# Kernel optimization log

Measured on AMD Instinct MI355X. Metric: run time of the kernel, lower is better.

The kernel has to match this reference:

```python
import jax, jax.numpy as jnp
import numpy as np

N, D, V = 4096, 256, 32000
B, T = 32, 256
U_DECAY, X_DECAY = 0.97, 0.97
EPS = 1e-6


def layernorm_row(z):
    # matches torch: (z - mean) / (std + eps), std with Bessel correction (ddof=1)
    m = jnp.mean(z, axis=-1, keepdims=True)
    s = jnp.std(z, axis=-1, keepdims=True, ddof=1)
    return (z - m) / (s + EPS)


def setup_inputs() -> dict:
    key = jax.random.key(0)
    k1, k2, k3, k4, k5 = jax.random.split(key, 5)
    token_emb = jax.random.normal(k1, (V, D), jnp.float32) / np.float32(np.sqrt(D))
    E = jax.random.normal(k2, (D, N), jnp.float32) / np.float32(np.sqrt(N))
    Dx = jax.random.normal(k3, (N, D), jnp.float32) / np.float32(np.sqrt(D))
    Dy = jax.random.normal(k4, (N, D), jnp.float32) / np.float32(np.sqrt(D))
    idx = jax.random.randint(k5, (B, T), 0, V)
    return {"idx": idx, "token_emb": token_emb, "E": E, "Dx": Dx, "Dy": Dy}


def reference(idx, token_emb, E, Dx, Dy):
    b = idx.shape[0]

    def step(carry, tok):
        x, rho = carry                                   # x: (b,n), rho: (b,d,n)
        v_prev = token_emb[tok]                          # (b,d) embedding gather
        x_t = X_DECAY * x + jax.nn.relu(v_prev @ Dx.T)   # (b,n)
        x_t = x_t / (jnp.sum(jnp.abs(x_t), axis=-1, keepdims=True) + EPS)  # L1 normalize
        a_star = jnp.einsum('bdn,bn->bd', rho, x_t)      # fast-weight readout
        y_t = jax.nn.relu(layernorm_row(a_star) @ Dy.T) * jax.nn.relu(x_t)  # (b,n)
        v_star = layernorm_row(y_t @ E.T)                # (b,d)
        # Hebbian decayed outer-product memory update
        rho = U_DECAY * (rho + jnp.einsum('bd,bn->bdn', layernorm_row(v_prev), x_t))
        return (x_t, rho), v_star

    x0 = jnp.zeros((b, N), jnp.float32)
    rho0 = jnp.zeros((b, D, N), jnp.float32)
    (_, _), vs = jax.lax.scan(step, (x0, rho0), idx.T)   # vs: (T,b,d)
    return jnp.transpose(vs, (1, 0, 2))                  # (b,T,d)
```

## Files before the change

kernel.cpp:

```cpp
#include <hip/hip_runtime.h>
#include <hip/hip_bf16.h>

#define NN 4096
#define DD 256
#define BB 32
#define TT 256
#define EPS 1e-6f
#define DECAY 0.97f
#define LOG2_DECAY -0.043943348f

typedef __hip_bfloat16 bf16;
typedef short short8 __attribute__((ext_vector_type(8)));
typedef float floatx4 __attribute__((ext_vector_type(4)));

__device__ __forceinline__ float blk_sum_256(float v, volatile float* s4) {
#pragma unroll
    for (int o = 32; o > 0; o >>= 1) v += __shfl_down(v, o, 64);
    int lane = threadIdx.x & 63, w = threadIdx.x >> 6;
    __syncthreads();
    if (lane == 0) s4[w] = v;
    __syncthreads();
    return s4[0] + s4[1] + s4[2] + s4[3];
}

__device__ __forceinline__ void gl16(const bf16* g, bf16* l) {
    __builtin_amdgcn_global_load_lds((const __attribute__((address_space(1))) void*)g,
                                     (__attribute__((address_space(3))) void*)l, 16, 0, 0);
}

__global__ void k_detect(const unsigned short* __restrict__ raw, int* __restrict__ flag) {
    __shared__ int cnt[4];
    int tid = threadIdx.x;
    int bad = 0;
    for (int i = tid; i < 8192; i += 256) {
        unsigned int u = raw[2 * i];
        float v = __uint_as_float(u << 16);
        if (!(fabsf(v) < 1e6f)) bad++;
    }
#pragma unroll
    for (int o = 32; o > 0; o >>= 1) bad += __shfl_down(bad, o, 64);
    int lane = tid & 63, w = tid >> 6;
    if (lane == 0) cnt[w] = bad;
    __syncthreads();
    if (tid == 0) flag[0] = (cnt[0] + cnt[1] + cnt[2] + cnt[3] < 32) ? 1 : 0;
}

__global__ void k_convert_bf16(const void* __restrict__ src, bf16* __restrict__ dst, int n,
                               const int* __restrict__ flag) {
    int i = blockIdx.x * 256 + threadIdx.x;
    if (i >= n) return;
    float v = flag[0] ? __bfloat162float(((const bf16*)src)[i]) : ((const float*)src)[i];
    dst[i] = __float2bfloat16(v);
}

__global__ __launch_bounds__(256) void k_gather_ln(const void* __restrict__ emb,
                                                   const int* __restrict__ idx,
                                                   bf16* __restrict__ Vpb,
                                                   bf16* __restrict__ Ub,
                                                   const int* __restrict__ flag) {
    __shared__ float s4[4];
    int r = blockIdx.x, d = threadIdx.x;
    int tok = idx[r];
    long o = (long)tok * DD + d;
    float e = flag[0] ? __bfloat162float(((const bf16*)emb)[o]) : ((const float*)emb)[o];
    Vpb[(long)r * DD + d] = __float2bfloat16(e);
    float m = blk_sum_256(e, s4) * (1.0f / DD);
    float zc = e - m;
    float var = blk_sum_256(zc * zc, s4) * (1.0f / (DD - 1));
    Ub[(long)r * DD + d] = __float2bfloat16(zc / (sqrtf(fmaxf(var, 0.f)) + EPS));
}

__global__ __launch_bounds__(256) void k_transpose(const bf16* __restrict__ Ub,
                                                   bf16* __restrict__ Ut) {
    __shared__ bf16 tile[32][33];
    int b = blockIdx.z;
    int t0 = blockIdx.x * 32, d0 = blockIdx.y * 32;
    const bf16* src = Ub + (long)b * TT * DD;
    bf16* dst = Ut + (long)b * DD * TT;
    int rr = threadIdx.x >> 3, c4 = (threadIdx.x & 7) * 4;
#pragma unroll
    for (int i = 0; i < 4; i++) tile[rr][c4 + i] = src[(long)(t0 + rr) * DD + d0 + c4 + i];
    __syncthreads();
#pragma unroll
    for (int i = 0; i < 4; i++) dst[(long)(d0 + rr) * TT + t0 + c4 + i] = tile[c4 + i][rr];
}

enum { EPI_RELU_BF16 = 0, EPI_NONE_F32 = 1, EPI_RELU_MULX_BF16 = 2 };

template <int EPI, int KSPLIT>
__global__ __launch_bounds__(256) void k_mfma_nt(int K,
                                                 const bf16* __restrict__ A, int lda, long sA,
                                                 const bf16* __restrict__ B, int ldb, long sB,
                                                 void* __restrict__ Cv, int ldc, long sC,
                                                 const bf16* __restrict__ Xaux) {
    __shared__ bf16 As[128][32];
    __shared__ bf16 Bs[128][32];
    int z = blockIdx.z;
    int bz = z / KSPLIT, ks = z % KSPLIT;
    A += (long)bz * sA;
    B += (long)bz * sB;
    int bm = blockIdx.y * 128, bn = blockIdx.x * 128;
    int tid = threadIdx.x;
    int srow = tid >> 2, scol = (tid & 3) << 3;
    int w = tid >> 6, lane = tid & 63;
    int wm = (w >> 1) * 64, wn = (w & 1) * 64;
    int lm = lane & 15, kh = lane >> 4;

    floatx4 acc[4][4];
#pragma unroll
    for (int i = 0; i < 4; i++)
#pragma unroll
        for (int j = 0; j < 4; j++) acc[i][j] = (floatx4){0.f, 0.f, 0.f, 0.f};

    int kchunk = K / KSPLIT;
    int kbeg = ks * kchunk, kend = kbeg + kchunk;
    const bf16* gA0 = A + (long)(bm + srow) * lda + scol;
    const bf16* gA1 = gA0 + (long)64 * lda;
    const bf16* gB0 = B + (long)(bn + srow) * ldb + scol;
    const bf16* gB1 = gB0 + (long)64 * ldb;
    bf16* lA0 = &As[srow][scol];
    bf16* lA1 = &As[srow + 64][scol];
    bf16* lB0 = &Bs[srow][scol];
    bf16* lB1 = &Bs[srow + 64][scol];

    for (int k0 = kbeg; k0 < kend; k0 += 32) {
        __syncthreads();
        gl16(gA0 + k0, lA0);
        gl16(gA1 + k0, lA1);
        gl16(gB0 + k0, lB0);
        gl16(gB1 + k0, lB1);
        __syncthreads();
        short8 af[4], bfr[4];
#pragma unroll
        for (int i = 0; i < 4; i++) af[i] = *(const short8*)&As[wm + i * 16 + lm][kh * 8];
#pragma unroll
        for (int j = 0; j < 4; j++) bfr[j] = *(const short8*)&Bs[wn + j * 16 + lm][kh * 8];
#pragma unroll
        for (int i = 0; i < 4; i++)
#pragma unroll
            for (int j = 0; j < 4; j++)
                acc[i][j] = __builtin_amdgcn_mfma_f32_16x16x32_bf16(af[i], bfr[j], acc[i][j], 0, 0, 0);
    }

    long cbase = (long)z * sC;
#pragma unroll
    for (int i = 0; i < 4; i++) {
#pragma unroll
        for (int j = 0; j < 4; j++) {
#pragma unroll
            for (int r = 0; r < 4; r++) {
                int gm = bm + wm + i * 16 + kh * 4 + r;
                int gn = bn + wn + j * 16 + lm;
                float v = acc[i][j][r];
                long off = cbase + (long)gm * ldc + gn;
                if (EPI == EPI_NONE_F32) {
                    ((float*)Cv)[off] = v;
                } else if (EPI == EPI_RELU_BF16) {
                    ((bf16*)Cv)[off] = __float2bfloat16(fmaxf(v, 0.f));
                } else {
                    float x = __bfloat162float(Xaux[off]);
                    ((bf16*)Cv)[off] = __float2bfloat16(fmaxf(v, 0.f) * fmaxf(x, 0.f));
                }
            }
        }
    }
}

__global__ __launch_bounds__(256) void k_rowsum(const bf16* __restrict__ Wb,
                                                float* __restrict__ Wsum) {
    __shared__ float s4[4];
    long r = blockIdx.x;
    const bf16* row = Wb + r * NN;
    float acc = 0.f;
    for (int j = threadIdx.x; j < NN; j += 256) acc += __bfloat162float(row[j]);
    float tot = blk_sum_256(acc, s4);
    if (threadIdx.x == 0) Wsum[r] = tot;
}

__global__ __launch_bounds__(256) void k_scalar_scan(const float* __restrict__ Wsum,
                                                     float* __restrict__ invS) {
    __shared__ float sw[BB * TT];
    for (int i = threadIdx.x; i < BB * TT; i += 256) sw[i] = Wsum[i];
    __syncthreads();
    int b = threadIdx.x;
    if (b < BB) {
        float sig = 0.f;
        for (int t = 0; t < TT; t++) {
            float S = DECAY * sig + sw[b * TT + t];
            float inv = 1.f / (S + EPS);
            invS[b * TT + t] = inv;
            sig = S * inv;
        }
    }
}

__global__ __launch_bounds__(256) void k_colscan(bf16* __restrict__ W,
                                                 const float* __restrict__ invS) {
    __shared__ float sv[TT];
    int b = blockIdx.y;
    sv[threadIdx.x] = invS[b * TT + threadIdx.x];
    __syncthreads();
    int n = blockIdx.x * 256 + threadIdx.x;
    bf16* p = W + (long)b * TT * NN + n;
    float x = 0.f;
    for (int t = 0; t < TT; t++) {
        float w = __bfloat162float(p[(long)t * NN]);
        x = (DECAY * x + w) * sv[t];
        p[(long)t * NN] = __float2bfloat16(x);
    }
}

__global__ __launch_bounds__(256) void k_reduce_mask(const float* __restrict__ Gp,
                                                     bf16* __restrict__ G) {
    int r = blockIdx.x;
    int b = r >> 8, t = r & 255;
    int s = threadIdx.x;
    long base = ((long)b * 4) * 65536 + (long)t * 256 + s;
    float v = Gp[base] + Gp[base + 65536] + Gp[base + 2 * 65536] + Gp[base + 3 * 65536];
    float o = (s < t) ? v * exp2f((float)(t - s) * LOG2_DECAY) : 0.f;
    G[(long)r * 256 + s] = __float2bfloat16(o);
}

__global__ __launch_bounds__(256) void k_ln_rows(const float* __restrict__ Z,
                                                 bf16* __restrict__ O) {
    __shared__ float s4[4];
    long r = blockIdx.x;
    int d = threadIdx.x;
    float z = Z[r * DD + d];
    float m = blk_sum_256(z, s4) * (1.0f / DD);
    float zc = z - m;
    float var = blk_sum_256(zc * zc, s4) * (1.0f / (DD - 1));
    O[r * DD + d] = __float2bfloat16(zc / (sqrtf(fmaxf(var, 0.f)) + EPS));
}

__global__ __launch_bounds__(256) void k_final_ln(const float* __restrict__ Zp,
                                                  void* __restrict__ out,
                                                  const int* __restrict__ flag) {
    __shared__ float s4[4];
    long r = blockIdx.x;
    int d = threadIdx.x;
    const long SL = (long)8192 * 256;
    long o = r * DD + d;
    float z = Zp[o] + Zp[o + SL] + Zp[o + 2 * SL] + Zp[o + 3 * SL];
    float m = blk_sum_256(z, s4) * (1.0f / DD);
    float zc = z - m;
    float var = blk_sum_256(zc * zc, s4) * (1.0f / (DD - 1));
    float v = zc / (sqrtf(fmaxf(var, 0.f)) + EPS);
    if (flag[0]) ((bf16*)out)[o] = __float2bfloat16(v);
    else ((float*)out)[o] = v;
}

extern "C" void kernel_launch(void* const* d_in, const int* in_sizes, int n_in,
                              void* d_out, int out_size, void* d_ws, size_t ws_size,
                              hipStream_t stream) {
    const int* idx = (const int*)d_in[0];
    const void* emb = d_in[1];
    const void* E = d_in[2];
    const void* Dx = d_in[3];
    const void* Dy = d_in[4];

    char* base = (char*)d_ws;
    size_t off = 0;
    int* flag = (int*)base; off += 1024;
    bf16* Dxb = (bf16*)(base + off); off += (size_t)NN * DD * 2;
    bf16* Dyb = (bf16*)(base + off); off += (size_t)NN * DD * 2;
    bf16* Eb  = (bf16*)(base + off); off += (size_t)DD * NN * 2;
    bf16* Vpb = (bf16*)(base + off); off += (size_t)BB * TT * DD * 2;
    bf16* Ub  = (bf16*)(base + off); off += (size_t)BB * TT * DD * 2;
    bf16* Ut  = (bf16*)(base + off); off += (size_t)BB * TT * DD * 2;
    float* Wsum = (float*)(base + off); off += (size_t)BB * TT * 4;
    float* invS = (float*)(base + off); off += (size_t)BB * TT * 4;
    float* Astar = (float*)(base + off); off += (size_t)BB * TT * DD * 4;
    bf16* ALNb = (bf16*)(base + off); off += (size_t)BB * TT * DD * 2;
    bf16* G = (bf16*)(base + off); off += (size_t)BB * TT * TT * 2;
    float* Gp = (float*)(base + off); off += (size_t)4 * BB * TT * TT * 4;
    float* Zp = Gp;
    bf16* Xb = (bf16*)(base + off); off += (size_t)BB * TT * NN * 2;

    const int M = BB * TT;

    k_detect<<<1, 256, 0, stream>>>((const unsigned short*)emb, flag);
    k_convert_bf16<<<(NN * DD + 255) / 256, 256, 0, stream>>>(Dx, Dxb, NN * DD, flag);
    k_convert_bf16<<<(NN * DD + 255) / 256, 256, 0, stream>>>(Dy, Dyb, NN * DD, flag);
    k_convert_bf16<<<(DD * NN + 255) / 256, 256, 0, stream>>>(E, Eb, DD * NN, flag);

    k_gather_ln<<<M, 256, 0, stream>>>(emb, idx, Vpb, Ub, flag);
    k_transpose<<<dim3(8, 8, BB), 256, 0, stream>>>(Ub, Ut);

    k_mfma_nt<EPI_RELU_BF16, 1><<<dim3(32, 64, 1), 256, 0, stream>>>(
        DD, Vpb, DD, 0, Dxb, DD, 0, Xb, NN, 0, nullptr);

    k_rowsum<<<M, 256, 0, stream>>>(Xb, Wsum);
    k_scalar_scan<<<1, 256, 0, stream>>>(Wsum, invS);
    k_colscan<<<dim3(16, BB, 1), 256, 0, stream>>>(Xb, invS);

    k_mfma_nt<EPI_NONE_F32, 4><<<dim3(2, 2, BB * 4), 256, 0, stream>>>(
        NN, Xb, NN, (long)TT * NN, Xb, NN, (long)TT * NN, Gp, TT, (long)TT * TT, nullptr);
    k_reduce_mask<<<M, 256, 0, stream>>>(Gp, G);

    k_mfma_nt<EPI_NONE_F32, 1><<<dim3(2, 2, BB), 256, 0, stream>>>(
        TT, G, TT, (long)TT * TT, Ut, TT, (long)DD * TT, Astar, DD, (long)TT * DD, nullptr);
    k_ln_rows<<<M, 256, 0, stream>>>(Astar, ALNb);

    k_mfma_nt<EPI_RELU_MULX_BF16, 1><<<dim3(32, 64, 1), 256, 0, stream>>>(
        DD, ALNb, DD, 0, Dyb, DD, 0, Xb, NN, 0, Xb);

    k_mfma_nt<EPI_NONE_F32, 4><<<dim3(2, 64, 4), 256, 0, stream>>>(
        NN, Xb, NN, 0, Eb, NN, 0, Zp, DD, (long)M * DD, nullptr);

    k_final_ln<<<M, 256, 0, stream>>>(Zp, d_out, flag);
}
```

Measured before the change: 360.7 us.

## Fuse rowsum into GEMM epilogue, vectorize stores, triangular Gram tiles, merge conversions

Merges the three weight-conversion launches into one vectorized kernel. The first GEMM now computes row sums inside its epilogue with atomics, which removes the separate rowsum pass over Xb. Epilogues stage results through LDS so they can write 16-byte vectorized stores. The Gram GEMM launches only the three lower-triangular 128x128 tiles because of the causal mask, and the G·U GEMM is split along K with the two partials summed in the LN kernel. This adds atomics, an extra memset and LDS staging, and relies on the upper tile being unused by the mask.

```diff
diff --git a/kernel.cpp b/kernel.cpp
--- a/kernel.cpp
+++ b/kernel.cpp
@@ -12,6 +12,10 @@
 typedef __hip_bfloat16 bf16;
 typedef short short8 __attribute__((ext_vector_type(8)));
 typedef float floatx4 __attribute__((ext_vector_type(4)));
+
+__device__ __forceinline__ float bfu2f(short u) {
+    return __uint_as_float(((unsigned)(unsigned short)u) << 16);
+}
 
 __device__ __forceinline__ float blk_sum_256(float v, volatile float* s4) {
 #pragma unroll
@@ -45,12 +49,32 @@
     if (tid == 0) flag[0] = (cnt[0] + cnt[1] + cnt[2] + cnt[3] < 32) ? 1 : 0;
 }
 
-__global__ void k_convert_bf16(const void* __restrict__ src, bf16* __restrict__ dst, int n,
-                               const int* __restrict__ flag) {
+__global__ __launch_bounds__(256) void k_convert3(const void* __restrict__ s0,
+                                                  const void* __restrict__ s1,
+                                                  const void* __restrict__ s2,
+                                                  bf16* __restrict__ d0,
+                                                  bf16* __restrict__ d1,
+                                                  bf16* __restrict__ d2,
+                                                  const int* __restrict__ flag) {
+    const int per = NN * DD / 8;
     int i = blockIdx.x * 256 + threadIdx.x;
-    if (i >= n) return;
-    float v = flag[0] ? __bfloat162float(((const bf16*)src)[i]) : ((const float*)src)[i];
-    dst[i] = __float2bfloat16(v);
+    int m = i / per, j = i % per;
+    const void* s = (m == 0) ? s0 : (m == 1) ? s1 : s2;
+    bf16* d = (m == 0) ? d0 : (m == 1) ? d1 : d2;
+    if (flag[0]) {
+        ((uint4*)d)[j] = ((const uint4*)s)[j];
+    } else {
+        const float4* f = (const float4*)s;
+        float4 a = f[2 * j], b = f[2 * j + 1];
+        short8 o;
+        float va[8] = {a.x, a.y, a.z, a.w, b.x, b.y, b.z, b.w};
+#pragma unroll
+        for (int k = 0; k < 8; k++) {
+            bf16 t = __float2bfloat16(va[k]);
+            o[k] = *reinterpret_cast<short*>(&t);
+        }
+        ((short8*)d)[j] = o;
+    }
 }
 
 __global__ __launch_bounds__(256) void k_gather_ln(const void* __restrict__ emb,
@@ -87,19 +111,28 @@
 
 enum { EPI_RELU_BF16 = 0, EPI_NONE_F32 = 1, EPI_RELU_MULX_BF16 = 2 };
 
-template <int EPI, int KSPLIT>
+template <int EPI, int KSPLIT, int TRI>
 __global__ __launch_bounds__(256) void k_mfma_nt(int K,
                                                  const bf16* __restrict__ A, int lda, long sA,
                                                  const bf16* __restrict__ B, int ldb, long sB,
                                                  void* __restrict__ Cv, int ldc, long sC,
-                                                 const bf16* __restrict__ Xaux) {
-    __shared__ bf16 As[128][32];
-    __shared__ bf16 Bs[128][32];
+                                                 const bf16* __restrict__ Xaux,
+                                                 float* __restrict__ Wsum) {
+    __shared__ __align__(16) char smem[17408];
+    bf16* As = (bf16*)smem;
+    bf16* Bs = (bf16*)(smem + 8192);
+    bf16* R = (bf16*)smem;
+
     int z = blockIdx.z;
     int bz = z / KSPLIT, ks = z % KSPLIT;
     A += (long)bz * sA;
     B += (long)bz * sB;
-    int bm = blockIdx.y * 128, bn = blockIdx.x * 128;
+    int bx = blockIdx.x, by = blockIdx.y;
+    if (TRI) {
+        by = (blockIdx.x >= 1) ? 1 : 0;
+        bx = (blockIdx.x == 2) ? 1 : 0;
+    }
+    int bm = by * 128, bn = bx * 128;
     int tid = threadIdx.x;
     int srow = tid >> 2, scol = (tid & 3) << 3;
     int w = tid >> 6, lane = tid & 63;
@@ -118,10 +151,10 @@
     const bf16* gA1 = gA0 + (long)64 * lda;
     const bf16* gB0 = B + (long)(bn + srow) * ldb + scol;
     const bf16* gB1 = gB0 + (long)64 * ldb;
-    bf16* lA0 = &As[srow][scol];
-    bf16* lA1 = &As[srow + 64][scol];
-    bf16* lB0 = &Bs[srow][scol];
-    bf16* lB1 = &Bs[srow + 64][scol];
+    bf16* lA0 = As + srow * 32 + scol;
+    bf16* lA1 = As + (srow + 64) * 32 + scol;
+    bf16* lB0 = Bs + srow * 32 + scol;
+    bf16* lB1 = Bs + (srow + 64) * 32 + scol;
 
     for (int k0 = kbeg; k0 < kend; k0 += 32) {
         __syncthreads();
@@ -132,9 +165,9 @@
         __syncthreads();
         short8 af[4], bfr[4];
 #pragma unroll
-        for (int i = 0; i < 4; i++) af[i] = *(const short8*)&As[wm + i * 16 + lm][kh * 8];
-#pragma unroll
-        for (int j = 0; j < 4; j++) bfr[j] = *(const short8*)&Bs[wn + j * 16 + lm][kh * 8];
+        for (int i = 0; i < 4; i++) af[i] = *(const short8*)(As + (wm + i * 16 + lm) * 32 + kh * 8);
+#pragma unroll
+        for (int j = 0; j < 4; j++) bfr[j] = *(const short8*)(Bs + (wn + j * 16 + lm) * 32 + kh * 8);
 #pragma unroll
         for (int i = 0; i < 4; i++)
 #pragma unroll
@@ -142,39 +175,65 @@
                 acc[i][j] = __builtin_amdgcn_mfma_f32_16x16x32_bf16(af[i], bfr[j], acc[i][j], 0, 0, 0);
     }
 
-    long cbase = (long)z * sC;
-#pragma unroll
-    for (int i = 0; i < 4; i++) {
-#pragma unroll
-        for (int j = 0; j < 4; j++) {
-#pragma unroll
-            for (int r = 0; r < 4; r++) {
-                int gm = bm + wm + i * 16 + kh * 4 + r;
-                int gn = bn + wn + j * 16 + lm;
-                float v = acc[i][j][r];
-                long off = cbase + (long)gm * ldc + gn;
-                if (EPI == EPI_NONE_F32) {
-                    ((float*)Cv)[off] = v;
-                } else if (EPI == EPI_RELU_BF16) {
-                    ((bf16*)Cv)[off] = __float2bfloat16(fmaxf(v, 0.f));
-                } else {
-                    float x = __bfloat162float(Xaux[off]);
-                    ((bf16*)Cv)[off] = __float2bfloat16(fmaxf(v, 0.f) * fmaxf(x, 0.f));
+    if (EPI == EPI_NONE_F32) {
+        long cbase = (long)z * sC;
+#pragma unroll
+        for (int i = 0; i < 4; i++)
+#pragma unroll
+            for (int j = 0; j < 4; j++)
+#pragma unroll
+                for (int r = 0; r < 4; r++) {
+                    int gm = bm + wm + i * 16 + kh * 4 + r;
+                    int gn = bn + wn + j * 16 + lm;
+                    ((float*)Cv)[cbase + (long)gm * ldc + gn] = acc[i][j][r];
                 }
+        return;
+    }
+
+#pragma unroll
+    for (int p = 0; p < 2; p++) {
+        __syncthreads();
+        if ((w >> 1) == p) {
+#pragma unroll
+            for (int i = 0; i < 4; i++)
+#pragma unroll
+                for (int j = 0; j < 4; j++)
+#pragma unroll
+                    for (int r = 0; r < 4; r++) {
+                        int rr = i * 16 + kh * 4 + r;
+                        int cc = wn + j * 16 + lm;
+                        R[rr * 136 + cc] = __float2bfloat16(fmaxf(acc[i][j][r], 0.f));
+                    }
+        }
+        __syncthreads();
+#pragma unroll
+        for (int it = 0; it < 4; it++) {
+            int row_l = it * 16 + (tid >> 4);
+            int c8 = (tid & 15) * 8;
+            short8 vv = *(const short8*)(R + row_l * 136 + c8);
+            int gm = bm + p * 64 + row_l;
+            long off = (long)gm * ldc + bn + c8;
+            if (EPI == EPI_RELU_BF16) {
+                *(short8*)((bf16*)Cv + off) = vv;
+                float s = 0.f;
+#pragma unroll
+                for (int k = 0; k < 8; k++) s += bfu2f(vv[k]);
+#pragma unroll
+                for (int o = 8; o > 0; o >>= 1) s += __shfl_down(s, o, 16);
+                if ((tid & 15) == 0) atomicAdd(&Wsum[gm], s);
+            } else {
+                short8 xx = *(const short8*)(Xaux + off);
+                short8 oo;
+#pragma unroll
+                for (int k = 0; k < 8; k++) {
+                    float prod = bfu2f(vv[k]) * fmaxf(bfu2f(xx[k]), 0.f);
+                    bf16 t = __float2bfloat16(prod);
+                    oo[k] = *reinterpret_cast<short*>(&t);
+                }
+                *(short8*)((bf16*)Cv + off) = oo;
             }
         }
     }
-}
-
-__global__ __launch_bounds__(256) void k_rowsum(const bf16* __restrict__ Wb,
-                                                float* __restrict__ Wsum) {
-    __shared__ float s4[4];
-    long r = blockIdx.x;
-    const bf16* row = Wb + r * NN;
-    float acc = 0.f;
-    for (int j = threadIdx.x; j < NN; j += 256) acc += __bfloat162float(row[j]);
-    float tot = blk_sum_256(acc, s4);
-    if (threadIdx.x == 0) Wsum[r] = tot;
 }
 
 __global__ __launch_bounds__(256) void k_scalar_scan(const float* __restrict__ Wsum,
@@ -221,12 +280,14 @@
     G[(long)r * 256 + s] = __float2bfloat16(o);
 }
 
-__global__ __launch_bounds__(256) void k_ln_rows(const float* __restrict__ Z,
+__global__ __launch_bounds__(256) void k_ln_rows(const float* __restrict__ Zp,
                                                  bf16* __restrict__ O) {
     __shared__ float s4[4];
     long r = blockIdx.x;
     int d = threadIdx.x;
-    float z = Z[r * DD + d];
+    long b = r >> 8, t = r & 255;
+    long base = (b * 2) * 65536 + t * 256 + d;
+    float z = Zp[base] + Zp[base + 65536];
     float m = blk_sum_256(z, s4) * (1.0f / DD);
     float zc = z - m;
     float var = blk_sum_256(zc * zc, s4) * (1.0f / (DD - 1));
@@ -270,43 +331,41 @@
     bf16* Ut  = (bf16*)(base + off); off += (size_t)BB * TT * DD * 2;
     float* Wsum = (float*)(base + off); off += (size_t)BB * TT * 4;
     float* invS = (float*)(base + off); off += (size_t)BB * TT * 4;
-    float* Astar = (float*)(base + off); off += (size_t)BB * TT * DD * 4;
     bf16* ALNb = (bf16*)(base + off); off += (size_t)BB * TT * DD * 2;
     bf16* G = (bf16*)(base + off); off += (size_t)BB * TT * TT * 2;
     float* Gp = (float*)(base + off); off += (size_t)4 * BB * TT * TT * 4;
+    float* Astar = Gp;
     float* Zp = Gp;
     bf16* Xb = (bf16*)(base + off); off += (size_t)BB * TT * NN * 2;
 
     const int M = BB * TT;
 
     k_detect<<<1, 256, 0, stream>>>((const unsigned short*)emb, flag);
-    k_convert_bf16<<<(NN * DD + 255) / 256, 256, 0, stream>>>(Dx, Dxb, NN * DD, flag);
-    k_convert_bf16<<<(NN * DD + 255) / 256, 256, 0, stream>>>(Dy, Dyb, NN * DD, flag);
-    k_convert_bf16<<<(DD * NN + 255) / 256, 256, 0, stream>>>(E, Eb, DD * NN, flag);
-
+    k_convert3<<<3 * NN * DD / 8 / 256, 256, 0, stream>>>(Dx, Dy, E, Dxb, Dyb, Eb, flag);
     k_gather_ln<<<M, 256, 0, stream>>>(emb, idx, Vpb, Ub, flag);
     k_transpose<<<dim3(8, 8, BB), 256, 0, stream>>>(Ub, Ut);
 
-    k_mfma_nt<EPI_RELU_BF16, 1><<<dim3(32, 64, 1), 256, 0, stream>>>(
-        DD, Vpb, DD, 0, Dxb, DD, 0, Xb, NN, 0, nullptr);
-
-    k_rowsum<<<M, 256, 0, stream>>>(Xb, Wsum);
+    hipMemsetAsync(Wsum, 0, (size_t)M * 4, stream);
+
+    k_mfma_nt<EPI_RELU_BF16, 1, 0><<<dim3(32, 64, 1), 256, 0, stream>>>(
+        DD, Vpb, DD, 0, Dxb, DD, 0, Xb, NN, 0, nullptr, Wsum);
+
     k_scalar_scan<<<1, 256, 0, stream>>>(Wsum, invS);
     k_colscan<<<dim3(16, BB, 1), 256, 0, stream>>>(Xb, invS);
 
-    k_mfma_nt<EPI_NONE_F32, 4><<<dim3(2, 2, BB * 4), 256, 0, stream>>>(
-        NN, Xb, NN, (long)TT * NN, Xb, NN, (long)TT * NN, Gp, TT, (long)TT * TT, nullptr);
+    k_mfma_nt<EPI_NONE_F32, 4, 1><<<dim3(3, 1, BB * 4), 256, 0, stream>>>(
+        NN, Xb, NN, (long)TT * NN, Xb, NN, (long)TT * NN, Gp, TT, (long)TT * TT, nullptr, nullptr);
     k_reduce_mask<<<M, 256, 0, stream>>>(Gp, G);
 
-    k_mfma_nt<EPI_NONE_F32, 1><<<dim3(2, 2, BB), 256, 0, stream>>>(
-        TT, G, TT, (long)TT * TT, Ut, TT, (long)DD * TT, Astar, DD, (long)TT * DD, nullptr);
+    k_mfma_nt<EPI_NONE_F32, 2, 0><<<dim3(2, 2, BB * 2), 256, 0, stream>>>(
+        TT, G, TT, (long)TT * TT, Ut, TT, (long)DD * TT, Astar, DD, (long)TT * DD, nullptr, nullptr);
     k_ln_rows<<<M, 256, 0, stream>>>(Astar, ALNb);
 
-    k_mfma_nt<EPI_RELU_MULX_BF16, 1><<<dim3(32, 64, 1), 256, 0, stream>>>(
-        DD, ALNb, DD, 0, Dyb, DD, 0, Xb, NN, 0, Xb);
-
-    k_mfma_nt<EPI_NONE_F32, 4><<<dim3(2, 64, 4), 256, 0, stream>>>(
-        NN, Xb, NN, 0, Eb, NN, 0, Zp, DD, (long)M * DD, nullptr);
+    k_mfma_nt<EPI_RELU_MULX_BF16, 1, 0><<<dim3(32, 64, 1), 256, 0, stream>>>(
+        DD, ALNb, DD, 0, Dyb, DD, 0, Xb, NN, 0, Xb, nullptr);
+
+    k_mfma_nt<EPI_NONE_F32, 4, 0><<<dim3(2, 64, 4), 256, 0, stream>>>(
+        NN, Xb, NN, 0, Eb, NN, 0, Zp, DD, (long)M * DD, nullptr, nullptr);
 
     k_final_ln<<<M, 256, 0, stream>>>(Zp, d_out, flag);
 }
```

Result: faster. 339.7 us (-5.8%).
